# Kernel tuning notes

Measured on AMD Instinct MI355X. Metric: run time of the kernel, lower is better.

Reference implementation:

```python
import jax, jax.numpy as jnp
import numpy as np

BN_EPS = 1e-5
KS = 4  # 4x4 morphology kernel (np.ones((4,4)))


def _bn(x, gamma, beta, mean, var):
    # eval-mode BatchNorm2d over channel dim 1 of [B,C,H,W]
    inv = jax.lax.rsqrt(var + BN_EPS)
    return (x - mean[None, :, None, None]) * (gamma * inv)[None, :, None, None] + beta[None, :, None, None]


def _erosion_to_dilate(m):
    # m: [B,1,H,W]; threshold > 0.3, then 4x4 binary erosion (min-pool) and
    # dilation (max-pool), SAME padding; border padded so it does not erode/dilate,
    # matching cv2's default morphology border behavior.
    z = jnp.where(m > 0.3, 1.0, 0.0).astype(m.dtype)
    er = jax.lax.reduce_window(z, jnp.array(1.0, z.dtype), jax.lax.min,
                               (1, 1, KS, KS), (1, 1, 1, 1), 'SAME')
    di = jax.lax.reduce_window(z, jnp.array(0.0, z.dtype), jax.lax.max,
                               (1, 1, KS, KS), (1, 1, 1, 1), 'SAME')
    # [maske, background, maskd] along channel dim -> [B,3,H,W]
    return jnp.concatenate([er, 1.0 - di, di - er], axis=1)


def setup_inputs() -> dict:
    key = jax.random.key(0)
    ks = jax.random.split(key, 8)
    B, C, H, W = 8, 256, 128, 128
    feature = jax.random.normal(ks[0], (B, C, H, W), dtype=jnp.float32)
    m = jax.random.uniform(ks[1], (B, 1, H, W), dtype=jnp.float32)
    w_feat = jax.random.normal(ks[2], (C, C), dtype=jnp.float32) * 0.02
    w_out = jax.random.normal(ks[3], (C, 2 * C), dtype=jnp.float32) * 0.02
    bn_f_gamma = jnp.ones((C,), jnp.float32)
    bn_f_beta = jnp.zeros((C,), jnp.float32)
    bn_f_mean = jnp.zeros((C,), jnp.float32)
    bn_f_var = jnp.ones((C,), jnp.float32)
    bn_o_gamma = jnp.ones((C,), jnp.float32)
    bn_o_beta = jnp.zeros((C,), jnp.float32)
    bn_o_mean = jnp.zeros((C,), jnp.float32)
    bn_o_var = jnp.ones((C,), jnp.float32)
    return {"feature": feature, "m": m, "w_feat": w_feat,
            "bn_f_gamma": bn_f_gamma, "bn_f_beta": bn_f_beta,
            "bn_f_mean": bn_f_mean, "bn_f_var": bn_f_var,
            "w_out": w_out, "bn_o_gamma": bn_o_gamma, "bn_o_beta": bn_o_beta,
            "bn_o_mean": bn_o_mean, "bn_o_var": bn_o_var}


def reference(feature, m, w_feat, bn_f_gamma, bn_f_beta, bn_f_mean, bn_f_var,
              w_out, bn_o_gamma, bn_o_beta, bn_o_mean, bn_o_var):
    B, C, H, W = feature.shape
    HW = H * W
    m = jax.nn.relu(m)
    # erosion_to_dilate is computed via numpy/OpenCV in the original -> detached
    fbu = jax.lax.stop_gradient(_erosion_to_dilate(m)).reshape(B, 3, HW)
    f1 = feature.reshape(B, C, HW)
    # mid_feature = fbu @ feature^T : [B,3,C]
    mid = jnp.einsum('bkn,bcn->bkc', fbu, f1)
    # conv1x1_feature: 1x1 conv (no bias) + eval BN, NO relu (BasicConv2d.forward)
    cf = _bn(jnp.einsum('bchw,oc->bohw', feature, w_feat),
             bn_f_gamma, bn_f_beta, bn_f_mean, bn_f_var).reshape(B, C, HW)
    mid1 = jnp.einsum('bkc,bcn->bkn', mid, cf)          # [B,3,HW]
    mid2 = jnp.einsum('bkc,bkn->bcn', mid, mid1)        # [B,C,HW]
    mid2 = mid2.reshape(B, C, H, W)
    cat = jnp.concatenate([feature, mid2], axis=1)      # [B,2C,H,W]
    out = _bn(jnp.einsum('bchw,oc->bohw', cat, w_out),
              bn_o_gamma, bn_o_beta, bn_o_mean, bn_o_var)
    return out
```

## Files before the change

### kernel.cpp

```cpp
#include <hip/hip_runtime.h>

#define HW 16384
#define LDSP 66

typedef unsigned short ushort_t;
typedef unsigned int uint32;
typedef __attribute__((ext_vector_type(8))) short short8;
typedef __attribute__((ext_vector_type(4))) float floatx4;

__device__ __forceinline__ ushort_t f2bf(float x) {
  uint32 u = __float_as_uint(x);
  u += 0x7fffu + ((u >> 16) & 1u);
  return (ushort_t)(u >> 16);
}

__global__ __launch_bounds__(256) void k_masks(const float* __restrict__ m,
                                               float* __restrict__ er,
                                               float* __restrict__ di) {
  int idx = blockIdx.x * 256 + threadIdx.x;
  int b = idx >> 14;
  int p = idx & (HW - 1);
  int i = p >> 7, j = p & 127;
  const float* mb = m + (b << 14);
  float ermn = 1.f, dimx = 0.f;
  for (int di_ = -1; di_ <= 2; ++di_) {
    int ii = i + di_;
    if (ii < 0 || ii >= 128) continue;
    for (int dj = -1; dj <= 2; ++dj) {
      int jj = j + dj;
      if (jj < 0 || jj >= 128) continue;
      float z = ((double)mb[ii * 128 + jj] > 0.3) ? 1.f : 0.f;
      ermn = fminf(ermn, z);
      dimx = fmaxf(dimx, z);
    }
  }
  er[idx] = ermn;
  di[idx] = dimx;
}

__global__ __launch_bounds__(256) void k_midsums(const float* __restrict__ f,
                                                 const float* __restrict__ er,
                                                 const float* __restrict__ di,
                                                 float* __restrict__ out) {
  int b = blockIdx.x >> 8;
  int c = blockIdx.x & 255;
  const float4* f4 = (const float4*)(f + ((size_t)(b * 256 + c) << 14));
  const float4* e4 = (const float4*)(er + ((size_t)b << 14));
  const float4* d4 = (const float4*)(di + ((size_t)b << 14));
  int t = threadIdx.x;
  float se = 0.f, st = 0.f, sd = 0.f;
#pragma unroll
  for (int it = 0; it < 16; ++it) {
    int i = it * 256 + t;
    float4 x = f4[i];
    float4 e = e4[i];
    float4 dd = d4[i];
    st += (x.x + x.y) + (x.z + x.w);
    se += x.x * e.x + x.y * e.y + x.z * e.z + x.w * e.w;
    sd += x.x * dd.x + x.y * dd.y + x.z * dd.z + x.w * dd.w;
  }
  __shared__ float red[3][4];
  for (int off = 32; off; off >>= 1) {
    se += __shfl_down(se, off);
    st += __shfl_down(st, off);
    sd += __shfl_down(sd, off);
  }
  int wave = t >> 6;
  if ((t & 63) == 0) { red[0][wave] = se; red[1][wave] = st; red[2][wave] = sd; }
  __syncthreads();
  if (t == 0) {
    se = red[0][0] + red[0][1] + red[0][2] + red[0][3];
    st = red[1][0] + red[1][1] + red[1][2] + red[1][3];
    sd = red[2][0] + red[2][1] + red[2][2] + red[2][3];
    float* o = out + (size_t)(b * 256 + c) * 3;
    o[0] = se; o[1] = st; o[2] = sd;
  }
}

__global__ __launch_bounds__(256) void k_prep(
    const float* __restrict__ midsums, const float* __restrict__ wfeat,
    const float* __restrict__ gf, const float* __restrict__ bfp,
    const float* __restrict__ mfp, const float* __restrict__ vfp,
    const float* __restrict__ wout, const float* __restrict__ g2,
    const float* __restrict__ b2p, const float* __restrict__ m2p,
    const float* __restrict__ v2p, ushort_t* __restrict__ Wbf,
    float* __restrict__ bias_eff) {
  const int b = blockIdx.x;
  const int t = threadIdx.x;
  __shared__ float mid[3][256];
  __shared__ float msc[3][256];
  __shared__ float tl[256], s2l[256], t2l[256];
  __shared__ float ul[3];
  __shared__ float Bm[3][256];
  __shared__ float bias2[256];
  __shared__ float A2[256][3];

  {
    const float* ms = midsums + (size_t)(b * 256 + t) * 3;
    float se = ms[0], st = ms[1], sd = ms[2];
    float m0 = se, m1 = st - sd, m2v = sd - se;
    mid[0][t] = m0; mid[1][t] = m1; mid[2][t] = m2v;
    float s = gf[t] * rsqrtf(vfp[t] + 1e-5f);
    tl[t] = bfp[t] - mfp[t] * s;
    msc[0][t] = m0 * s; msc[1][t] = m1 * s; msc[2][t] = m2v * s;
    float s2 = g2[t] * rsqrtf(v2p[t] + 1e-5f);
    s2l[t] = s2;
    t2l[t] = b2p[t] - m2p[t] * s2;
  }
  __syncthreads();
  if (t < 3) {
    float u = 0.f;
#pragma unroll 8
    for (int c = 0; c < 256; ++c) u += mid[t][c] * tl[c];
    ul[t] = u;
  }
  {
    float b0 = 0.f, b1 = 0.f, b2v = 0.f;
#pragma unroll 8
    for (int o = 0; o < 256; ++o) {
      float wfv = wfeat[o * 256 + t];
      b0 += msc[0][o] * wfv;
      b1 += msc[1][o] * wfv;
      b2v += msc[2][o] * wfv;
    }
    Bm[0][t] = b0; Bm[1][t] = b1; Bm[2][t] = b2v;
  }
  __syncthreads();
  bias2[t] = mid[0][t] * ul[0] + mid[1][t] * ul[1] + mid[2][t] * ul[2];
  __syncthreads();
  {
    const float4* w2 = (const float4*)(wout + t * 512 + 256);
    float a0 = 0.f, a1 = 0.f, a2v = 0.f, bb = 0.f;
#pragma unroll 4
    for (int cq = 0; cq < 64; ++cq) {
      float4 wv = w2[cq];
      int c = cq * 4;
      a0 += wv.x * mid[0][c] + wv.y * mid[0][c + 1] + wv.z * mid[0][c + 2] + wv.w * mid[0][c + 3];
      a1 += wv.x * mid[1][c] + wv.y * mid[1][c + 1] + wv.z * mid[1][c + 2] + wv.w * mid[1][c + 3];
      a2v += wv.x * mid[2][c] + wv.y * mid[2][c + 1] + wv.z * mid[2][c + 2] + wv.w * mid[2][c + 3];
      bb += wv.x * bias2[c] + wv.y * bias2[c + 1] + wv.z * bias2[c + 2] + wv.w * bias2[c + 3];
    }
    A2[t][0] = a0; A2[t][1] = a1; A2[t][2] = a2v;
    bias_eff[b * 256 + t] = s2l[t] * bb + t2l[t];
  }
  __syncthreads();
  {
    float bm0 = Bm[0][t], bm1 = Bm[1][t], bm2 = Bm[2][t];
    ushort_t* Wb = Wbf + ((size_t)b << 16);
#pragma unroll 8
    for (int o = 0; o < 256; ++o) {
      float wv = wout[o * 512 + t];
      float val = s2l[o] * (wv + A2[o][0] * bm0 + A2[o][1] * bm1 + A2[o][2] * bm2);
      Wb[o * 256 + t] = f2bf(val);
    }
  }
}

__global__ __launch_bounds__(256) void k_gemm(const float* __restrict__ f,
                                              const ushort_t* __restrict__ Wbf,
                                              const float* __restrict__ bias,
                                              float* __restrict__ out) {
  __shared__ float lds[64 * LDSP];
  const int b = blockIdx.x >> 8;
  const int n0 = (blockIdx.x & 255) * 64;
  const int t = threadIdx.x;
  const int wv = t >> 6;
  const int lane = t & 63;
  const int l15 = lane & 15;
  const int quad = lane >> 4;
  const int obase = wv * 64;
  const float* fb = f + ((size_t)b << 22);
  const ushort_t* Wb = Wbf + ((size_t)b << 16);
  const float* biasb = bias + (b << 8);

  const int c_loc = t >> 2;
  const int f4c = t & 3;

  floatx4 acc[4][4];
#pragma unroll
  for (int ot = 0; ot < 4; ++ot) {
#pragma unroll
    for (int r = 0; r < 4; ++r) {
      float bv = biasb[obase + ot * 16 + quad * 4 + r];
#pragma unroll
      for (int nt = 0; nt < 4; ++nt) acc[ot][nt][r] = bv;
    }
  }

  for (int kc = 0; kc < 256; kc += 64) {
    const float4* gsrc = (const float4*)(fb + (size_t)(kc + c_loc) * HW + n0);
    float4 v[4];
#pragma unroll
    for (int k = 0; k < 4; ++k) v[k] = gsrc[f4c + 4 * k];
    if (kc) __syncthreads();
    float* dst = &lds[c_loc * LDSP];
#pragma unroll
    for (int k = 0; k < 4; ++k) {
      int col = (f4c + 4 * k) * 4;
      *(float2*)(dst + col) = make_float2(v[k].x, v[k].y);
      *(float2*)(dst + col + 2) = make_float2(v[k].z, v[k].w);
    }
    __syncthreads();
#pragma unroll
    for (int ks = 0; ks < 2; ++ks) {
      short8 a[4];
#pragma unroll
      for (int ot = 0; ot < 4; ++ot)
        a[ot] = *(const short8*)(Wb + (size_t)(obase + ot * 16 + l15) * 256 +
                                 kc + ks * 32 + quad * 8);
      short8 bfr[4];
#pragma unroll
      for (int nt = 0; nt < 4; ++nt) {
#pragma unroll
        for (int j = 0; j < 8; ++j)
          bfr[nt][j] = (short)f2bf(lds[(ks * 32 + quad * 8 + j) * LDSP + nt * 16 + l15]);
      }
#pragma unroll
      for (int ot = 0; ot < 4; ++ot)
#pragma unroll
        for (int nt = 0; nt < 4; ++nt)
          acc[ot][nt] = __builtin_amdgcn_mfma_f32_16x16x32_bf16(a[ot], bfr[nt], acc[ot][nt], 0, 0, 0);
    }
  }

  float* ob = out + ((size_t)b << 22);
#pragma unroll
  for (int ot = 0; ot < 4; ++ot)
#pragma unroll
    for (int nt = 0; nt < 4; ++nt)
#pragma unroll
      for (int r = 0; r < 4; ++r)
        ob[(size_t)(obase + ot * 16 + quad * 4 + r) * HW + n0 + nt * 16 + l15] = acc[ot][nt][r];
}

extern "C" void kernel_launch(void* const* d_in, const int* in_sizes, int n_in,
                              void* d_out, int out_size, void* d_ws, size_t ws_size,
                              hipStream_t stream) {
  (void)in_sizes; (void)n_in; (void)out_size; (void)ws_size;
  const float* feature = (const float*)d_in[0];
  const float* m = (const float*)d_in[1];
  const float* w_feat = (const float*)d_in[2];
  const float* gf = (const float*)d_in[3];
  const float* bf = (const float*)d_in[4];
  const float* mf = (const float*)d_in[5];
  const float* vf = (const float*)d_in[6];
  const float* w_out = (const float*)d_in[7];
  const float* g2 = (const float*)d_in[8];
  const float* b2 = (const float*)d_in[9];
  const float* m2 = (const float*)d_in[10];
  const float* v2 = (const float*)d_in[11];
  float* out = (float*)d_out;

  char* wsb = (char*)d_ws;
  float* er = (float*)wsb;
  float* di = (float*)(wsb + (512 << 10));
  float* midsums = (float*)(wsb + (1 << 20));
  float* bias_eff = (float*)(wsb + (1 << 20) + (32 << 10));
  ushort_t* Wbf = (ushort_t*)(wsb + (2 << 20));

  hipLaunchKernelGGL(k_masks, dim3(512), dim3(256), 0, stream, m, er, di);
  hipLaunchKernelGGL(k_midsums, dim3(2048), dim3(256), 0, stream, feature, er, di, midsums);
  hipLaunchKernelGGL(k_prep, dim3(8), dim3(256), 0, stream, midsums, w_feat,
                     gf, bf, mf, vf, w_out, g2, b2, m2, v2, Wbf, bias_eff);
  hipLaunchKernelGGL(k_gemm, dim3(2048), dim3(256), 0, stream, feature, Wbf, bias_eff, out);
}
```

Before: 341.8 us.

## Split prep kernel across more threads/blocks and store bf16-transposed tile in GEMM LDS

The 8-block prep kernel is split in two. The first kernel uses 1024 threads and reduces partial sums. A new 256-block kernel then builds the per-batch bf16 weight matrix, replacing a long serial loop that ran on only 8 blocks. The GEMM now converts feature values to bf16 once while writing them transposed into LDS, so B fragments load as single 16-byte vectors instead of eight scalar loads plus conversions per MFMA fragment. The transposed scalar LDS stores may cause bank conflicts, and the change adds one extra kernel launch.

```diff
diff --git a/kernel.cpp b/kernel.cpp
--- a/kernel.cpp
+++ b/kernel.cpp
@@ -1,7 +1,7 @@
 #include <hip/hip_runtime.h>
 
 #define HW 16384
-#define LDSP 66
+#define TP 72
 
 typedef unsigned short ushort_t;
 typedef unsigned int uint32;
@@ -77,25 +77,30 @@
   }
 }
 
-__global__ __launch_bounds__(256) void k_prep(
+__global__ __launch_bounds__(1024) void k_prep_a(
     const float* __restrict__ midsums, const float* __restrict__ wfeat,
     const float* __restrict__ gf, const float* __restrict__ bfp,
     const float* __restrict__ mfp, const float* __restrict__ vfp,
     const float* __restrict__ wout, const float* __restrict__ g2,
     const float* __restrict__ b2p, const float* __restrict__ m2p,
-    const float* __restrict__ v2p, ushort_t* __restrict__ Wbf,
-    float* __restrict__ bias_eff) {
+    const float* __restrict__ v2p, float* __restrict__ BmW,
+    float* __restrict__ A2W, float* __restrict__ bias_eff) {
   const int b = blockIdx.x;
-  const int t = threadIdx.x;
+  const int tid = threadIdx.x;
+  const int t = tid & 255;
+  const int part = tid >> 8;
   __shared__ float mid[3][256];
   __shared__ float msc[3][256];
-  __shared__ float tl[256], s2l[256], t2l[256];
+  __shared__ float tl[256];
+  __shared__ float s2l[256], t2l[256];
+  __shared__ float bias2[256];
+  __shared__ float ulp[3][4];
   __shared__ float ul[3];
-  __shared__ float Bm[3][256];
-  __shared__ float bias2[256];
-  __shared__ float A2[256][3];
-
-  {
+  __shared__ float Bmp[4][3][256];
+  __shared__ float A2p[4][256][3];
+  __shared__ float bbp[4][256];
+
+  if (part == 0) {
     const float* ms = midsums + (size_t)(b * 256 + t) * 3;
     float se = ms[0], st = ms[1], sd = ms[2];
     float m0 = se, m1 = st - sd, m2v = sd - se;
@@ -111,28 +116,36 @@
   if (t < 3) {
     float u = 0.f;
 #pragma unroll 8
-    for (int c = 0; c < 256; ++c) u += mid[t][c] * tl[c];
-    ul[t] = u;
+    for (int c = part * 64; c < part * 64 + 64; ++c) u += mid[t][c] * tl[c];
+    ulp[t][part] = u;
   }
   {
     float b0 = 0.f, b1 = 0.f, b2v = 0.f;
 #pragma unroll 8
-    for (int o = 0; o < 256; ++o) {
+    for (int o = part * 64; o < part * 64 + 64; ++o) {
       float wfv = wfeat[o * 256 + t];
       b0 += msc[0][o] * wfv;
       b1 += msc[1][o] * wfv;
       b2v += msc[2][o] * wfv;
     }
-    Bm[0][t] = b0; Bm[1][t] = b1; Bm[2][t] = b2v;
-  }
-  __syncthreads();
-  bias2[t] = mid[0][t] * ul[0] + mid[1][t] * ul[1] + mid[2][t] * ul[2];
+    Bmp[part][0][t] = b0; Bmp[part][1][t] = b1; Bmp[part][2][t] = b2v;
+  }
+  __syncthreads();
+  if (tid < 3) ul[tid] = ulp[tid][0] + ulp[tid][1] + ulp[tid][2] + ulp[tid][3];
+  if (part == 0) {
+#pragma unroll
+    for (int k = 0; k < 3; ++k)
+      BmW[b * 768 + k * 256 + t] =
+          Bmp[0][k][t] + Bmp[1][k][t] + Bmp[2][k][t] + Bmp[3][k][t];
+  }
+  __syncthreads();
+  if (part == 0) bias2[t] = mid[0][t] * ul[0] + mid[1][t] * ul[1] + mid[2][t] * ul[2];
   __syncthreads();
   {
     const float4* w2 = (const float4*)(wout + t * 512 + 256);
     float a0 = 0.f, a1 = 0.f, a2v = 0.f, bb = 0.f;
 #pragma unroll 4
-    for (int cq = 0; cq < 64; ++cq) {
+    for (int cq = part * 16; cq < part * 16 + 16; ++cq) {
       float4 wv = w2[cq];
       int c = cq * 4;
       a0 += wv.x * mid[0][c] + wv.y * mid[0][c + 1] + wv.z * mid[0][c + 2] + wv.w * mid[0][c + 3];
@@ -140,19 +153,48 @@
       a2v += wv.x * mid[2][c] + wv.y * mid[2][c + 1] + wv.z * mid[2][c + 2] + wv.w * mid[2][c + 3];
       bb += wv.x * bias2[c] + wv.y * bias2[c + 1] + wv.z * bias2[c + 2] + wv.w * bias2[c + 3];
     }
-    A2[t][0] = a0; A2[t][1] = a1; A2[t][2] = a2v;
+    A2p[part][t][0] = a0; A2p[part][t][1] = a1; A2p[part][t][2] = a2v;
+    bbp[part][t] = bb;
+  }
+  __syncthreads();
+  if (part == 0) {
+#pragma unroll
+    for (int k = 0; k < 3; ++k)
+      A2W[(size_t)(b * 256 + t) * 3 + k] =
+          A2p[0][t][k] + A2p[1][t][k] + A2p[2][t][k] + A2p[3][t][k];
+    float bb = bbp[0][t] + bbp[1][t] + bbp[2][t] + bbp[3][t];
     bias_eff[b * 256 + t] = s2l[t] * bb + t2l[t];
   }
-  __syncthreads();
-  {
-    float bm0 = Bm[0][t], bm1 = Bm[1][t], bm2 = Bm[2][t];
-    ushort_t* Wb = Wbf + ((size_t)b << 16);
-#pragma unroll 8
-    for (int o = 0; o < 256; ++o) {
-      float wv = wout[o * 512 + t];
-      float val = s2l[o] * (wv + A2[o][0] * bm0 + A2[o][1] * bm1 + A2[o][2] * bm2);
-      Wb[o * 256 + t] = f2bf(val);
-    }
+}
+
+__global__ __launch_bounds__(256) void k_wbuild(
+    const float* __restrict__ wout, const float* __restrict__ g2,
+    const float* __restrict__ v2p, const float* __restrict__ BmW,
+    const float* __restrict__ A2W, ushort_t* __restrict__ Wbf) {
+  const int b = blockIdx.x >> 5;
+  const int og = blockIdx.x & 31;
+  const int t = threadIdx.x;
+  __shared__ float s2o[8];
+  __shared__ float a2s[8][3];
+  float bm0 = BmW[b * 768 + t];
+  float bm1 = BmW[b * 768 + 256 + t];
+  float bm2 = BmW[b * 768 + 512 + t];
+  if (t < 8) {
+    int o = og * 8 + t;
+    s2o[t] = g2[o] * rsqrtf(v2p[o] + 1e-5f);
+  }
+  if (t < 24) {
+    int i = t / 3, k = t % 3;
+    a2s[i][k] = A2W[(size_t)(b * 256 + og * 8 + i) * 3 + k];
+  }
+  __syncthreads();
+  ushort_t* Wb = Wbf + ((size_t)b << 16);
+#pragma unroll
+  for (int i = 0; i < 8; ++i) {
+    int o = og * 8 + i;
+    float wv = wout[o * 512 + t];
+    float val = s2o[i] * (wv + a2s[i][0] * bm0 + a2s[i][1] * bm1 + a2s[i][2] * bm2);
+    Wb[o * 256 + t] = f2bf(val);
   }
 }
 
@@ -160,7 +202,7 @@
                                               const ushort_t* __restrict__ Wbf,
                                               const float* __restrict__ bias,
                                               float* __restrict__ out) {
-  __shared__ float lds[64 * LDSP];
+  __shared__ __align__(16) ushort_t ldsT[64 * TP];
   const int b = blockIdx.x >> 8;
   const int n0 = (blockIdx.x & 255) * 64;
   const int t = threadIdx.x;
@@ -174,7 +216,7 @@
   const float* biasb = bias + (b << 8);
 
   const int c_loc = t >> 2;
-  const int f4c = t & 3;
+  const int nb = t & 3;
 
   floatx4 acc[4][4];
 #pragma unroll
@@ -191,14 +233,16 @@
     const float4* gsrc = (const float4*)(fb + (size_t)(kc + c_loc) * HW + n0);
     float4 v[4];
 #pragma unroll
-    for (int k = 0; k < 4; ++k) v[k] = gsrc[f4c + 4 * k];
+    for (int k = 0; k < 4; ++k) v[k] = gsrc[nb * 4 + k];
     if (kc) __syncthreads();
-    float* dst = &lds[c_loc * LDSP];
+    ushort_t* dst = ldsT + c_loc;
 #pragma unroll
     for (int k = 0; k < 4; ++k) {
-      int col = (f4c + 4 * k) * 4;
-      *(float2*)(dst + col) = make_float2(v[k].x, v[k].y);
-      *(float2*)(dst + col + 2) = make_float2(v[k].z, v[k].w);
+      int nr = nb * 16 + k * 4;
+      dst[(nr + 0) * TP] = f2bf(v[k].x);
+      dst[(nr + 1) * TP] = f2bf(v[k].y);
+      dst[(nr + 2) * TP] = f2bf(v[k].z);
+      dst[(nr + 3) * TP] = f2bf(v[k].w);
     }
     __syncthreads();
 #pragma unroll
@@ -210,11 +254,8 @@
                                  kc + ks * 32 + quad * 8);
       short8 bfr[4];
 #pragma unroll
-      for (int nt = 0; nt < 4; ++nt) {
-#pragma unroll
-        for (int j = 0; j < 8; ++j)
-          bfr[nt][j] = (short)f2bf(lds[(ks * 32 + quad * 8 + j) * LDSP + nt * 16 + l15]);
-      }
+      for (int nt = 0; nt < 4; ++nt)
+        bfr[nt] = *(const short8*)(ldsT + (nt * 16 + l15) * TP + ks * 32 + quad * 8);
 #pragma unroll
       for (int ot = 0; ot < 4; ++ot)
 #pragma unroll
@@ -256,11 +297,14 @@
   float* di = (float*)(wsb + (512 << 10));
   float* midsums = (float*)(wsb + (1 << 20));
   float* bias_eff = (float*)(wsb + (1 << 20) + (32 << 10));
+  float* BmW = (float*)(wsb + (1 << 20) + (64 << 10));
+  float* A2W = (float*)(wsb + (1 << 20) + (128 << 10));
   ushort_t* Wbf = (ushort_t*)(wsb + (2 << 20));
 
   hipLaunchKernelGGL(k_masks, dim3(512), dim3(256), 0, stream, m, er, di);
   hipLaunchKernelGGL(k_midsums, dim3(2048), dim3(256), 0, stream, feature, er, di, midsums);
-  hipLaunchKernelGGL(k_prep, dim3(8), dim3(256), 0, stream, midsums, w_feat,
-                     gf, bf, mf, vf, w_out, g2, b2, m2, v2, Wbf, bias_eff);
+  hipLaunchKernelGGL(k_prep_a, dim3(8), dim3(1024), 0, stream, midsums, w_feat,
+                     gf, bf, mf, vf, w_out, g2, b2, m2, v2, BmW, A2W, bias_eff);
+  hipLaunchKernelGGL(k_wbuild, dim3(256), dim3(256), 0, stream, w_out, g2, v2, BmW, A2W, Wbf);
   hipLaunchKernelGGL(k_gemm, dim3(2048), dim3(256), 0, stream, feature, Wbf, bias_eff, out);
 }
```

Result: faster. 316.0 us, median of 2 (-7.5%).
